# Kernel tuning notes

Hardware: AMD Instinct MI355X
Metric: run time of the kernel (lower is better)

## Reference

```python
import jax, jax.numpy as jnp
import numpy as np

N_NODES = 50000
N_EDGES = 800000
EPS = 1e-5


def _glorot(key, fan_in, fan_out):
    lim = np.sqrt(6.0 / (fan_in + fan_out))
    return jax.random.uniform(key, (fan_in, fan_out), jnp.float32, -lim, lim)


def setup_inputs() -> dict:
    key = jax.random.key(0)
    ks = jax.random.split(key, 16)
    x = jax.random.normal(ks[0], (N_NODES, 88), jnp.float32)
    edge_index = jax.random.randint(ks[1], (2, N_EDGES), 0, N_NODES, jnp.int64)
    dims = [(88, 70), (70, 60), (60, 50), (50, 60), (60, 70), (70, 88)]
    inp = {"x": x, "edge_index": edge_index}
    for i, (fi, fo) in enumerate(dims):
        inp[f"W{i+1}"] = _glorot(ks[2 + i], fi, fo)
        inp[f"b{i+1}"] = jnp.zeros((fo,), jnp.float32)
    # BatchNorm affine params for layers with bn: widths 70,60,60,70
    for i, w in enumerate([70, 60, 60, 70]):
        inp[f"g{i+1}"] = jnp.ones((w,), jnp.float32)
        inp[f"be{i+1}"] = jnp.zeros((w,), jnp.float32)
    return inp


def _gcn_norm(edge_index, n_nodes):
    # add self-loops, symmetric normalization: D^-1/2 (A+I) D^-1/2
    loop = jnp.arange(n_nodes, dtype=edge_index.dtype)
    src = jnp.concatenate([edge_index[0], loop])
    dst = jnp.concatenate([edge_index[1], loop])
    deg = jax.ops.segment_sum(jnp.ones_like(dst, jnp.float32), dst, num_segments=n_nodes)
    dis = jnp.where(deg > 0, jax.lax.rsqrt(deg), 0.0)
    norm = dis[src] * dis[dst]  # [E+N]
    return src, dst, norm


def _gcn(x, W, b, src, dst, norm, n_nodes):
    h = x @ W  # transform first (small out dim)
    msg = h[src] * norm[:, None]
    return jax.ops.segment_sum(msg, dst, num_segments=n_nodes) + b


def _bn(x, g, be):
    mu = jnp.mean(x, axis=0)
    var = jnp.mean(jnp.square(x - mu), axis=0)
    return g * (x - mu) * jax.lax.rsqrt(var + EPS) + be


def reference(x, edge_index, W1, b1, W2, b2, W3, b3, W4, b4, W5, b5, W6, b6,
              g1, be1, g2, be2, g3, be3, g4, be4):
    n = x.shape[0]
    src, dst, norm = _gcn_norm(edge_index, n)
    # encoder
    h = jax.nn.relu(_gcn(x, W1, b1, src, dst, norm, n))
    h = _bn(h, g1, be1)
    h = jax.nn.relu(_gcn(h, W2, b2, src, dst, norm, n))
    h = _bn(h, g2, be2)
    h = _gcn(h, W3, b3, src, dst, norm, n)
    # decoder
    h = jax.nn.relu(_gcn(h, W4, b4, src, dst, norm, n))
    h = _bn(h, g3, be3)
    h = jax.nn.relu(_gcn(h, W5, b5, src, dst, norm, n))
    h = _bn(h, g4, be4)
    h = _gcn(h, W6, b6, src, dst, norm, n)
    return h
```

## Files before the change

### kernel.cpp

```cpp
#include <hip/hip_runtime.h>
#include <hip/hip_bf16.h>

typedef unsigned int  uint_t;
typedef unsigned short ushort_t;

#define NN 50000
#define NE 800000
#define NBLK 196

static inline int cdiv(long long a, long long b) { return (int)((a + b - 1) / b); }

__device__ inline float bflo(uint_t u) { return __uint_as_float(u << 16); }
__device__ inline float bfhi(uint_t u) { return __uint_as_float(u & 0xffff0000u); }
__device__ inline uint_t packbf(float x, float y) {
    uint_t xu = __float_as_uint(x), yu = __float_as_uint(y);
    xu += 0x7fffu + ((xu >> 16) & 1u);
    yu += 0x7fffu + ((yu >> 16) & 1u);
    return (xu >> 16) | (yu & 0xffff0000u);
}
__device__ inline ushort_t packbf1(float x) {
    uint_t xu = __float_as_uint(x);
    xu += 0x7fffu + ((xu >> 16) & 1u);
    return (ushort_t)(xu >> 16);
}


__global__ void k_prep(int* __restrict__ deg, float* __restrict__ bnacc) {
    int i = blockIdx.x * blockDim.x + threadIdx.x;
    if (i < NN) deg[i] = 0;
    if (i < 768) bnacc[i] = 0.0f;
}

__global__ void k_hist(const int* __restrict__ dst, int* __restrict__ deg) {
    int e = blockIdx.x * blockDim.x + threadIdx.x;
    if (e < NE) {
        int d = dst[e];
        if ((unsigned)d < NN) atomicAdd(&deg[d], 1);
    }
}

__global__ void k_bsum(const int* __restrict__ deg, int* __restrict__ bsum) {
    __shared__ int l[256];
    int tid = threadIdx.x;
    int i = blockIdx.x * 256 + tid;
    l[tid] = (i < NN) ? deg[i] : 0;
    __syncthreads();
    for (int o = 128; o > 0; o >>= 1) {
        if (tid < o) l[tid] += l[tid + o];
        __syncthreads();
    }
    if (tid == 0) bsum[blockIdx.x] = l[0];
}

__global__ void k_bscan(const int* __restrict__ bsum, int* __restrict__ boff,
                        int* __restrict__ row_ptr) {
    __shared__ int l[256];
    int tid = threadIdx.x;
    int v = (tid < NBLK) ? bsum[tid] : 0;
    l[tid] = v;
    __syncthreads();
    for (int o = 1; o < 256; o <<= 1) {
        int t = (tid >= o) ? l[tid - o] : 0;
        __syncthreads();
        l[tid] += t;
        __syncthreads();
    }
    boff[tid] = l[tid] - v;
    if (tid == 255) row_ptr[NN] = l[255];
}

__global__ void k_rowptr(const int* __restrict__ deg, const int* __restrict__ boff,
                         int* __restrict__ row_ptr, int* __restrict__ cursor,
                         float* __restrict__ dis) {
    __shared__ int l[256];
    int tid = threadIdx.x;
    int i = blockIdx.x * 256 + tid;
    int v = (i < NN) ? deg[i] : 0;
    l[tid] = v;
    __syncthreads();
    for (int o = 1; o < 256; o <<= 1) {
        int t = (tid >= o) ? l[tid - o] : 0;
        __syncthreads();
        l[tid] += t;
        __syncthreads();
    }
    if (i < NN) {
        int excl = boff[blockIdx.x] + l[tid] - v;
        row_ptr[i] = excl;
        cursor[i] = excl;
        dis[i] = rsqrtf((float)(v + 1));
    }
}

__global__ void k_fill(const int* __restrict__ src, const int* __restrict__ dst,
                       const float* __restrict__ dis,
                       int* __restrict__ cursor, int2* __restrict__ cw) {
    int e = blockIdx.x * blockDim.x + threadIdx.x;
    if (e < NE) {
        int s = src[e], d = dst[e];
        if ((unsigned)s < NN && (unsigned)d < NN) {
            int p = atomicAdd(&cursor[d], 1);
            cw[p] = make_int2(s, __float_as_int(dis[s] * dis[d]));
        }
    }
}

struct FoldJob {
    const float* W; const float* b;
    const float* bnacc; const float* g; const float* be;
    float* Wp; float* bf;
    int FI, FO, in_bn, out_b;
};
struct FoldJobs { FoldJob j[4]; };

__global__ void k_fold(FoldJobs jobs) {
    FoldJob J = jobs.j[blockIdx.x];
    const int FI = J.FI, FO = J.FO;
    const int NT = (FO + 15) / 16, FOP = 16 * NT;
    __shared__ float scl[96], shl[96];
    int tid = threadIdx.x;
    if (J.in_bn) {
        if (tid < FI) {
            const float inv_n = 1.0f / NN;
            float mu = J.bnacc[tid] * inv_n;
            float va = J.bnacc[96 + tid] * inv_n - mu * mu;
            float r  = rsqrtf(va + 1e-5f);
            float sc = J.g[tid] * r;
            scl[tid] = sc;
            shl[tid] = J.be[tid] - mu * sc;
        }
        __syncthreads();
    }
    for (int idx = tid; idx < FI * FOP; idx += 256) {
        int k = idx / FOP, j = idx - k * FOP;
        float w = (j < FO) ? J.W[k * FO + j] : 0.0f;
        if (J.in_bn) w *= scl[k];
        J.Wp[(k >> 1) * 2 * FOP + 2 * j + (k & 1)] = w;
    }
    if (tid < FOP) {
        float a = (J.out_b && tid < FO) ? J.b[tid] : 0.0f;
        if (J.in_bn && tid < FO) {
            for (int k = 0; k < FI; ++k) a = fmaf(shl[k], J.W[k * FO + tid], a);
        }
        J.bf[tid] = a;
    }
}

template<int FI, int FO, int IN_BN, int IN_F32, int OUT_F32, int OUT_BN>
__global__ __launch_bounds__(256)
void k_dense(const void* __restrict__ Xv, const float* __restrict__ Wp,
             const float* __restrict__ biasf, void* __restrict__ Hv,
             float* __restrict__ bnst) {
    constexpr int NT  = (FO + 15) / 16;
    constexpr int FOP = 16 * NT;
    constexpr int FIP = FI + 2;
    constexpr int KP  = FI / 2;

    __shared__ __align__(16) float xs[64 * FIP];
    __shared__ float ls[96], lq[96];

    int tid = threadIdx.x;
    int node0 = blockIdx.x * 64;

    if (OUT_BN) {
        if (tid < 96) { ls[tid] = 0.0f; lq[tid] = 0.0f; }
    }

    if (IN_F32) {
        for (int idx = tid; idx < 64 * FI; idx += 256) {
            int r = idx / FI, c = idx - r * FI;
            int n = node0 + r;
            float v = (n < NN) ? ((const float*)Xv)[(size_t)n * FI + c] : 0.0f;
            if (IN_BN) v = fmaxf(v, 0.0f);
            xs[r * FIP + c] = v;
        }
    } else {
        for (int idx = tid; idx < 64 * KP; idx += 256) {
            int r = idx / KP, c2 = idx - r * KP;
            int n = node0 + r;
            uint_t u = (n < NN) ? ((const uint_t*)Xv)[(size_t)n * KP + c2] : 0u;
            float f0 = bflo(u), f1 = bfhi(u);
            if (IN_BN) { f0 = fmaxf(f0, 0.0f); f1 = fmaxf(f1, 0.0f); }
            xs[r * FIP + 2 * c2]     = f0;
            xs[r * FIP + 2 * c2 + 1] = f1;
        }
    }
    __syncthreads();

    int ng = tid >> 4;
    int cg = tid & 15;

    float acc[4][NT];
    #pragma unroll
    for (int i = 0; i < 4; ++i)
        #pragma unroll
        for (int t = 0; t < NT; ++t) acc[i][t] = biasf[cg + 16 * t];

    #pragma unroll 2
    for (int k = 0; k < FI; k += 2) {
        float2 xv[4];
        #pragma unroll
        for (int i = 0; i < 4; ++i)
            xv[i] = *(const float2*)&xs[(ng + 16 * i) * FIP + k];
        const float* wrow = &Wp[(k >> 1) * 2 * FOP];
        #pragma unroll
        for (int t = 0; t < NT; ++t) {
            float2 w = *(const float2*)&wrow[2 * (cg + 16 * t)];
            #pragma unroll
            for (int i = 0; i < 4; ++i)
                acc[i][t] = fmaf(xv[i].y, w.y, fmaf(xv[i].x, w.x, acc[i][t]));
        }
    }

    if (OUT_BN) {
        #pragma unroll
        for (int t = 0; t < NT; ++t) {
            int j = cg + 16 * t;
            if (j < FO) {
                float ps = 0.0f, pq = 0.0f;
                #pragma unroll
                for (int i = 0; i < 4; ++i) {
                    if (node0 + ng + 16 * i < NN) {
                        float r = fmaxf(acc[i][t], 0.0f);
                        ps += r; pq += r * r;
                    }
                }
                atomicAdd(&ls[j], ps);
                atomicAdd(&lq[j], pq);
            }
        }
        __syncthreads();
        if (tid < FO) {
            atomicAdd(&bnst[tid], ls[tid]);
            atomicAdd(&bnst[96 + tid], lq[tid]);
        }
    }

    #pragma unroll
    for (int i = 0; i < 4; ++i) {
        int n = node0 + ng + 16 * i;
        if (n < NN) {
            #pragma unroll
            for (int t = 0; t < NT; ++t) {
                int j = cg + 16 * t;
                if (j < FO) {
                    if (OUT_F32) ((float*)Hv)[(size_t)n * FO + j] = acc[i][t];
                    else ((ushort_t*)Hv)[(size_t)n * FO + j] = packbf1(acc[i][t]);
                }
            }
        }
    }
}

template<int FO, int IN_BN, int OUT_BIAS, int OUT_BN>
__global__ void k_gather(const ushort_t* __restrict__ h, const int* __restrict__ row_ptr,
                         const int2* __restrict__ cw, const float* __restrict__ dis,
                         const float* __restrict__ bnacc, const float* __restrict__ g,
                         const float* __restrict__ be,
                         const float* __restrict__ b, ushort_t* __restrict__ A,
                         float* __restrict__ bnacc_out) {
    constexpr int F2 = FO / 2;
    __shared__ float ls[96], lq[96];
    int tid = threadIdx.x;
    if (OUT_BN) {
        if (tid < 96) { ls[tid] = 0.0f; lq[tid] = 0.0f; }
        __syncthreads();
    }

    int t0 = blockIdx.x * blockDim.x + tid;
    const int stride = gridDim.x * blockDim.x;
    int j2 = t0 % F2;
    int j = 2 * j2;

    float sc0 = 1.0f, sh0 = 0.0f, sc1 = 1.0f, sh1 = 0.0f;
    if (IN_BN) {
        const float inv_n = 1.0f / NN;
        float mu0 = bnacc[j] * inv_n;
        float va0 = bnacc[96 + j] * inv_n - mu0 * mu0;
        float r0  = rsqrtf(va0 + 1e-5f);
        sc0 = g[j] * r0; sh0 = be[j] - mu0 * sc0;
        float mu1 = bnacc[j + 1] * inv_n;
        float va1 = bnacc[96 + j + 1] * inv_n - mu1 * mu1;
        float r1  = rsqrtf(va1 + 1e-5f);
        sc1 = g[j + 1] * r1; sh1 = be[j + 1] - mu1 * sc1;
    }

    const uint_t* h2 = (const uint_t*)h + j2;
    float sx = 0.0f, qx = 0.0f, sy = 0.0f, qy = 0.0f;

    for (int t = t0; t < NN * F2; t += stride) {
        int i = t / F2;
        float di = dis[i];

        uint_t su = h2[(size_t)i * F2];
        float vx = bflo(su), vy = bfhi(su);
        if (IN_BN) { vx = fmaxf(vx, 0.0f) * sc0 + sh0; vy = fmaxf(vy, 0.0f) * sc1 + sh1; }
        float ax = vx * di * di;
        float ay = vy * di * di;

        int k = row_ptr[i], end = row_ptr[i + 1];

        for (; k + 16 <= end; k += 16) {
            uint_t uu[16]; float ww[16];
            #pragma unroll
            for (int q = 0; q < 16; ++q) {
                int2 c = cw[k + q];
                ww[q] = __int_as_float(c.y);
                uu[q] = h2[(size_t)c.x * F2];
            }
            #pragma unroll
            for (int q = 0; q < 16; ++q) {
                float tx = bflo(uu[q]), ty = bfhi(uu[q]);
                if (IN_BN) { tx = fmaxf(tx, 0.0f) * sc0 + sh0; ty = fmaxf(ty, 0.0f) * sc1 + sh1; }
                ax = fmaf(tx, ww[q], ax); ay = fmaf(ty, ww[q], ay);
            }
        }
        for (; k + 8 <= end; k += 8) {
            uint_t uu[8]; float ww[8];
            #pragma unroll
            for (int q = 0; q < 8; ++q) {
                int2 c = cw[k + q];
                ww[q] = __int_as_float(c.y);
                uu[q] = h2[(size_t)c.x * F2];
            }
            #pragma unroll
            for (int q = 0; q < 8; ++q) {
                float tx = bflo(uu[q]), ty = bfhi(uu[q]);
                if (IN_BN) { tx = fmaxf(tx, 0.0f) * sc0 + sh0; ty = fmaxf(ty, 0.0f) * sc1 + sh1; }
                ax = fmaf(tx, ww[q], ax); ay = fmaf(ty, ww[q], ay);
            }
        }
        for (; k + 4 <= end; k += 4) {
            uint_t uu[4]; float ww[4];
            #pragma unroll
            for (int q = 0; q < 4; ++q) {
                int2 c = cw[k + q];
                ww[q] = __int_as_float(c.y);
                uu[q] = h2[(size_t)c.x * F2];
            }
            #pragma unroll
            for (int q = 0; q < 4; ++q) {
                float tx = bflo(uu[q]), ty = bfhi(uu[q]);
                if (IN_BN) { tx = fmaxf(tx, 0.0f) * sc0 + sh0; ty = fmaxf(ty, 0.0f) * sc1 + sh1; }
                ax = fmaf(tx, ww[q], ax); ay = fmaf(ty, ww[q], ay);
            }
        }
        for (; k < end; ++k) {
            int2 c = cw[k];
            float w = __int_as_float(c.y);
            uint_t u = h2[(size_t)c.x * F2];
            float tx = bflo(u), ty = bfhi(u);
            if (IN_BN) { tx = fmaxf(tx, 0.0f) * sc0 + sh0; ty = fmaxf(ty, 0.0f) * sc1 + sh1; }
            ax = fmaf(tx, w, ax); ay = fmaf(ty, w, ay);
        }

        if (OUT_BIAS) { ax += b[j]; ay += b[j + 1]; }
        if (OUT_BN) {
            float rx = fmaxf(ax, 0.0f), ry = fmaxf(ay, 0.0f);
            sx += rx; qx += rx * rx;
            sy += ry; qy += ry * ry;
        }
        ((uint_t*)A)[(size_t)i * F2 + j2] = packbf(ax, ay);
    }

    if (OUT_BN) {
        atomicAdd(&ls[j], sx);     atomicAdd(&ls[j + 1], sy);
        atomicAdd(&lq[j], qx);     atomicAdd(&lq[j + 1], qy);
        __syncthreads();
        if (tid < FO) {
            atomicAdd(&bnacc_out[tid], ls[tid]);
            atomicAdd(&bnacc_out[96 + tid], lq[tid]);
        }
    }
}

extern "C" void kernel_launch(void* const* d_in, const int* in_sizes, int n_in,
                              void* d_out, int out_size, void* d_ws, size_t ws_size,
                              hipStream_t stream) {
    const float* x = (const float*)d_in[0];
    const int* ei = (const int*)d_in[1];
    const int* src = ei;
    const int* dst = ei + NE;
    const float* W1 = (const float*)d_in[2];  const float* b1 = (const float*)d_in[3];
    const float* W2 = (const float*)d_in[4];  const float* b2 = (const float*)d_in[5];
    const float* W3 = (const float*)d_in[6];  const float* b3 = (const float*)d_in[7];
    const float* W4 = (const float*)d_in[8];  const float* b4 = (const float*)d_in[9];
    const float* W5 = (const float*)d_in[10]; const float* b5 = (const float*)d_in[11];
    const float* W6 = (const float*)d_in[12]; const float* b6 = (const float*)d_in[13];
    const float* g1 = (const float*)d_in[14]; const float* be1 = (const float*)d_in[15];
    const float* g2 = (const float*)d_in[16]; const float* be2 = (const float*)d_in[17];
    const float* g3 = (const float*)d_in[18]; const float* be3 = (const float*)d_in[19];
    const float* g4 = (const float*)d_in[20]; const float* be4 = (const float*)d_in[21];

    int2* cw      = (int2*)d_ws;
    float* dis    = (float*)(cw + NE);
    float* bnacc  = dis + NN;
    float* Wp     = bnacc + 768;
    float* biasf  = Wp + 6 * 7040;
    int* deg      = (int*)(biasf + 6 * 96);
    int* row_ptr  = deg + NN;
    int* cursor   = row_ptr + NN + 1;
    int* bsum     = cursor + NN;
    int* boff     = bsum + 256;
    ushort_t* hB  = (ushort_t*)(boff + 256);
    ushort_t* aB  = hB + (size_t)NN * 70;
    float* out    = (float*)d_out;

    const int NB = 256;
    const int DGRID = cdiv(NN, 64);
    float* bn0 = bnacc;
    float* bn1 = bnacc + 192;
    float* bn2 = bnacc + 384;
    float* bn3 = bnacc + 576;
    float* WpL[6]; float* bfL[6];
    for (int i = 0; i < 6; ++i) { WpL[i] = Wp + i * 7040; bfL[i] = biasf + i * 96; }

    k_prep<<<cdiv(NN, NB), NB, 0, stream>>>(deg, bnacc);
    k_hist<<<cdiv(NE, NB), NB, 0, stream>>>(dst, deg);
    k_bsum<<<NBLK, 256, 0, stream>>>(deg, bsum);
    k_bscan<<<1, 256, 0, stream>>>(bsum, boff, row_ptr);
    k_rowptr<<<NBLK, 256, 0, stream>>>(deg, boff, row_ptr, cursor, dis);
    k_fill<<<cdiv(NE, NB), NB, 0, stream>>>(src, dst, dis, cursor, cw);

    {
        FoldJobs js;
        js.j[0] = {W1, nullptr, nullptr, nullptr, nullptr, WpL[0], bfL[0], 88, 70, 0, 0};
        js.j[1] = {W4, b4,      nullptr, nullptr, nullptr, WpL[3], bfL[3], 50, 60, 0, 1};
        js.j[2] = {W5, b5,      nullptr, nullptr, nullptr, WpL[4], bfL[4], 60, 70, 0, 1};
        js.j[3] = {W6, b6,      nullptr, nullptr, nullptr, WpL[5], bfL[5], 70, 88, 0, 1};
        k_fold<<<4, 256, 0, stream>>>(js);
    }

    k_dense<88, 70, 0, 1, 0, 0><<<DGRID, 256, 0, stream>>>(x, WpL[0], bfL[0], hB, nullptr);
    k_gather<70, 0, 1, 1><<<56 * 35, NB, 0, stream>>>(
        hB, row_ptr, cw, dis, nullptr, nullptr, nullptr, b1, aB, bn0);

    {
        FoldJobs js;
        js.j[0] = {W2, nullptr, bn0, g1, be1, WpL[1], bfL[1], 70, 60, 1, 0};
        k_fold<<<1, 256, 0, stream>>>(js);
    }
    k_dense<70, 60, 1, 0, 0, 0><<<DGRID, 256, 0, stream>>>(aB, WpL[1], bfL[1], hB, nullptr);
    k_gather<60, 0, 1, 1><<<56 * 30, NB, 0, stream>>>(
        hB, row_ptr, cw, dis, nullptr, nullptr, nullptr, b2, aB, bn1);

    {
        FoldJobs js;
        js.j[0] = {W3, nullptr, bn1, g2, be2, WpL[2], bfL[2], 60, 50, 1, 0};
        k_fold<<<1, 256, 0, stream>>>(js);
    }
    k_dense<60, 50, 1, 0, 0, 0><<<DGRID, 256, 0, stream>>>(aB, WpL[2], bfL[2], hB, nullptr);
    k_gather<50, 0, 1, 0><<<cdiv((long long)NN * 25, NB), NB, 0, stream>>>(
        hB, row_ptr, cw, dis, nullptr, nullptr, nullptr, b3, aB, nullptr);

    k_gather<50, 0, 0, 0><<<cdiv((long long)NN * 25, NB), NB, 0, stream>>>(
        aB, row_ptr, cw, dis, nullptr, nullptr, nullptr, nullptr, hB, nullptr);
    k_dense<50, 60, 0, 0, 0, 1><<<DGRID, 256, 0, stream>>>(hB, WpL[3], bfL[3], aB, bn2);

    k_gather<60, 1, 0, 0><<<cdiv((long long)NN * 30, NB), NB, 0, stream>>>(
        aB, row_ptr, cw, dis, bn2, g3, be3, nullptr, hB, nullptr);
    k_dense<60, 70, 0, 0, 0, 1><<<DGRID, 256, 0, stream>>>(hB, WpL[4], bfL[4], aB, bn3);

    k_gather<70, 1, 0, 0><<<cdiv((long long)NN * 35, NB), NB, 0, stream>>>(
        aB, row_ptr, cw, dis, bn3, g4, be4, nullptr, hB, nullptr);
    k_dense<70, 88, 0, 0, 1, 0><<<DGRID, 256, 0, stream>>>(hB, WpL[5], bfL[5], out, nullptr);
}
```

Before: 553.8 us.

## Chunk feature layout into 8 column slabs and compute edge weights on the fly

```diff
diff --git a/kernel.cpp b/kernel.cpp
--- a/kernel.cpp
+++ b/kernel.cpp
@@ -93,14 +93,13 @@
 }
 
 __global__ void k_fill(const int* __restrict__ src, const int* __restrict__ dst,
-                       const float* __restrict__ dis,
-                       int* __restrict__ cursor, int2* __restrict__ cw) {
+                       int* __restrict__ cursor, int* __restrict__ col) {
     int e = blockIdx.x * blockDim.x + threadIdx.x;
     if (e < NE) {
         int s = src[e], d = dst[e];
         if ((unsigned)s < NN && (unsigned)d < NN) {
             int p = atomicAdd(&cursor[d], 1);
-            cw[p] = make_int2(s, __float_as_int(dis[s] * dis[d]));
+            col[p] = s;
         }
     }
 }
@@ -146,7 +145,7 @@
     }
 }
 
-template<int FI, int FO, int IN_BN, int IN_F32, int OUT_F32, int OUT_BN>
+template<int FI, int FO, int IN_BN, int PRI, int PRO, int OUT_BN>
 __global__ __launch_bounds__(256)
 void k_dense(const void* __restrict__ Xv, const float* __restrict__ Wp,
              const float* __restrict__ biasf, void* __restrict__ Hv,
@@ -154,7 +153,6 @@
     constexpr int NT  = (FO + 15) / 16;
     constexpr int FOP = 16 * NT;
     constexpr int FIP = FI + 2;
-    constexpr int KP  = FI / 2;
 
     __shared__ __align__(16) float xs[64 * FIP];
     __shared__ float ls[96], lq[96];
@@ -166,7 +164,7 @@
         if (tid < 96) { ls[tid] = 0.0f; lq[tid] = 0.0f; }
     }
 
-    if (IN_F32) {
+    if (PRI == 0) {
         for (int idx = tid; idx < 64 * FI; idx += 256) {
             int r = idx / FI, c = idx - r * FI;
             int n = node0 + r;
@@ -175,14 +173,20 @@
             xs[r * FIP + c] = v;
         }
     } else {
-        for (int idx = tid; idx < 64 * KP; idx += 256) {
-            int r = idx / KP, c2 = idx - r * KP;
-            int n = node0 + r;
-            uint_t u = (n < NN) ? ((const uint_t*)Xv)[(size_t)n * KP + c2] : 0u;
+        constexpr int PRIc = PRI ? PRI : 1;
+        for (int idx = tid; idx < 8 * 64 * PRIc; idx += 256) {
+            int c   = idx / (64 * PRIc);
+            int rem = idx - c * 64 * PRIc;
+            int r   = rem / PRIc;
+            int p   = rem - r * PRIc;
+            int n   = node0 + r;
+            uint_t u = (n < NN)
+                ? ((const uint_t*)Xv)[(size_t)c * NN * PRIc + (size_t)n * PRIc + p] : 0u;
             float f0 = bflo(u), f1 = bfhi(u);
             if (IN_BN) { f0 = fmaxf(f0, 0.0f); f1 = fmaxf(f1, 0.0f); }
-            xs[r * FIP + 2 * c2]     = f0;
-            xs[r * FIP + 2 * c2 + 1] = f1;
+            int j = c * 2 * PRIc + 2 * p;
+            if (j < FI)     xs[r * FIP + j]     = f0;
+            if (j + 1 < FI) xs[r * FIP + j + 1] = f1;
         }
     }
     __syncthreads();
@@ -243,23 +247,30 @@
             #pragma unroll
             for (int t = 0; t < NT; ++t) {
                 int j = cg + 16 * t;
-                if (j < FO) {
-                    if (OUT_F32) ((float*)Hv)[(size_t)n * FO + j] = acc[i][t];
-                    else ((ushort_t*)Hv)[(size_t)n * FO + j] = packbf1(acc[i][t]);
+                if (PRO == 0) {
+                    if (j < FO) ((float*)Hv)[(size_t)n * FO + j] = acc[i][t];
+                } else {
+                    constexpr int PROc = PRO ? PRO : 1;
+                    int co = j / (2 * PROc);
+                    int w  = j - co * 2 * PROc;
+                    ((ushort_t*)Hv)[(size_t)co * NN * 2 * PROc + (size_t)n * 2 * PROc + w]
+                        = packbf1(acc[i][t]);
                 }
             }
         }
     }
 }
 
-template<int FO, int IN_BN, int OUT_BIAS, int OUT_BN>
-__global__ void k_gather(const ushort_t* __restrict__ h, const int* __restrict__ row_ptr,
-                         const int2* __restrict__ cw, const float* __restrict__ dis,
-                         const float* __restrict__ bnacc, const float* __restrict__ g,
-                         const float* __restrict__ be,
-                         const float* __restrict__ b, ushort_t* __restrict__ A,
-                         float* __restrict__ bnacc_out) {
-    constexpr int F2 = FO / 2;
+template<int FO, int PR, int IN_BN, int OUT_BIAS, int OUT_BN>
+__global__ __launch_bounds__(256)
+void k_gather(const uint_t* __restrict__ h, const int* __restrict__ row_ptr,
+              const int* __restrict__ col, const float* __restrict__ dis,
+              const float* __restrict__ bnacc, const float* __restrict__ g,
+              const float* __restrict__ be,
+              const float* __restrict__ b, uint_t* __restrict__ A,
+              float* __restrict__ bnacc_out) {
+    constexpr int NPB = 256 / PR;
+    constexpr int NBTOT = (NN + NPB - 1) / NPB;
     __shared__ float ls[96], lq[96];
     int tid = threadIdx.x;
     if (OUT_BN) {
@@ -267,36 +278,48 @@
         __syncthreads();
     }
 
-    int t0 = blockIdx.x * blockDim.x + tid;
-    const int stride = gridDim.x * blockDim.x;
-    int j2 = t0 % F2;
+    int chunk = blockIdx.x & 7;
+    int GB    = gridDim.x >> 3;
+    int ln = tid / PR, p = tid - ln * PR;
+    int j2 = chunk * PR + p;
     int j = 2 * j2;
 
-    float sc0 = 1.0f, sh0 = 0.0f, sc1 = 1.0f, sh1 = 0.0f;
+    float sc0 = 0.0f, sh0 = 0.0f, sc1 = 0.0f, sh1 = 0.0f;
     if (IN_BN) {
         const float inv_n = 1.0f / NN;
-        float mu0 = bnacc[j] * inv_n;
-        float va0 = bnacc[96 + j] * inv_n - mu0 * mu0;
-        float r0  = rsqrtf(va0 + 1e-5f);
-        sc0 = g[j] * r0; sh0 = be[j] - mu0 * sc0;
-        float mu1 = bnacc[j + 1] * inv_n;
-        float va1 = bnacc[96 + j + 1] * inv_n - mu1 * mu1;
-        float r1  = rsqrtf(va1 + 1e-5f);
-        sc1 = g[j + 1] * r1; sh1 = be[j + 1] - mu1 * sc1;
-    }
-
-    const uint_t* h2 = (const uint_t*)h + j2;
+        if (j < FO) {
+            float mu = bnacc[j] * inv_n;
+            float va = bnacc[96 + j] * inv_n - mu * mu;
+            float r  = rsqrtf(va + 1e-5f);
+            sc0 = g[j] * r; sh0 = be[j] - mu * sc0;
+        }
+        if (j + 1 < FO) {
+            float mu = bnacc[j + 1] * inv_n;
+            float va = bnacc[96 + j + 1] * inv_n - mu * mu;
+            float r  = rsqrtf(va + 1e-5f);
+            sc1 = g[j + 1] * r; sh1 = be[j + 1] - mu * sc1;
+        }
+    }
+    float bx = 0.0f, by = 0.0f;
+    if (OUT_BIAS) {
+        if (j < FO)     bx = b[j];
+        if (j + 1 < FO) by = b[j + 1];
+    }
+
+    const uint_t* hr = h + (size_t)chunk * NN * PR + p;
+    uint_t* Ar = A + (size_t)chunk * NN * PR + p;
     float sx = 0.0f, qx = 0.0f, sy = 0.0f, qy = 0.0f;
 
-    for (int t = t0; t < NN * F2; t += stride) {
-        int i = t / F2;
+    for (int nb = blockIdx.x >> 3; nb < NBTOT; nb += GB) {
+        int i = nb * NPB + ln;
+        if (ln >= NPB || i >= NN) continue;
         float di = dis[i];
 
-        uint_t su = h2[(size_t)i * F2];
+        uint_t su = hr[(size_t)i * PR];
         float vx = bflo(su), vy = bfhi(su);
         if (IN_BN) { vx = fmaxf(vx, 0.0f) * sc0 + sh0; vy = fmaxf(vy, 0.0f) * sc1 + sh1; }
-        float ax = vx * di * di;
-        float ay = vy * di * di;
+        float ax = vx * di * di + bx;
+        float ay = vy * di * di + by;
 
         int k = row_ptr[i], end = row_ptr[i + 1];
 
@@ -304,9 +327,9 @@
             uint_t uu[16]; float ww[16];
             #pragma unroll
             for (int q = 0; q < 16; ++q) {
-                int2 c = cw[k + q];
-                ww[q] = __int_as_float(c.y);
-                uu[q] = h2[(size_t)c.x * F2];
+                int c = col[k + q];
+                ww[q] = dis[c] * di;
+                uu[q] = hr[(size_t)c * PR];
             }
             #pragma unroll
             for (int q = 0; q < 16; ++q) {
@@ -319,9 +342,9 @@
             uint_t uu[8]; float ww[8];
             #pragma unroll
             for (int q = 0; q < 8; ++q) {
-                int2 c = cw[k + q];
-                ww[q] = __int_as_float(c.y);
-                uu[q] = h2[(size_t)c.x * F2];
+                int c = col[k + q];
+                ww[q] = dis[c] * di;
+                uu[q] = hr[(size_t)c * PR];
             }
             #pragma unroll
             for (int q = 0; q < 8; ++q) {
@@ -334,9 +357,9 @@
             uint_t uu[4]; float ww[4];
             #pragma unroll
             for (int q = 0; q < 4; ++q) {
-                int2 c = cw[k + q];
-                ww[q] = __int_as_float(c.y);
-                uu[q] = h2[(size_t)c.x * F2];
+                int c = col[k + q];
+                ww[q] = dis[c] * di;
+                uu[q] = hr[(size_t)c * PR];
             }
             #pragma unroll
             for (int q = 0; q < 4; ++q) {
@@ -346,26 +369,25 @@
             }
         }
         for (; k < end; ++k) {
-            int2 c = cw[k];
-            float w = __int_as_float(c.y);
-            uint_t u = h2[(size_t)c.x * F2];
+            int c = col[k];
+            float w = dis[c] * di;
+            uint_t u = hr[(size_t)c * PR];
             float tx = bflo(u), ty = bfhi(u);
             if (IN_BN) { tx = fmaxf(tx, 0.0f) * sc0 + sh0; ty = fmaxf(ty, 0.0f) * sc1 + sh1; }
             ax = fmaf(tx, w, ax); ay = fmaf(ty, w, ay);
         }
 
-        if (OUT_BIAS) { ax += b[j]; ay += b[j + 1]; }
         if (OUT_BN) {
             float rx = fmaxf(ax, 0.0f), ry = fmaxf(ay, 0.0f);
             sx += rx; qx += rx * rx;
             sy += ry; qy += ry * ry;
         }
-        ((uint_t*)A)[(size_t)i * F2 + j2] = packbf(ax, ay);
+        Ar[(size_t)i * PR] = packbf(ax, ay);
     }
 
     if (OUT_BN) {
-        atomicAdd(&ls[j], sx);     atomicAdd(&ls[j + 1], sy);
-        atomicAdd(&lq[j], qx);     atomicAdd(&lq[j + 1], qy);
+        if (j < FO)     { atomicAdd(&ls[j], sx);     atomicAdd(&lq[j], qx); }
+        if (j + 1 < FO) { atomicAdd(&ls[j + 1], sy); atomicAdd(&lq[j + 1], qy); }
         __syncthreads();
         if (tid < FO) {
             atomicAdd(&bnacc_out[tid], ls[tid]);
@@ -392,8 +414,8 @@
     const float* g3 = (const float*)d_in[18]; const float* be3 = (const float*)d_in[19];
     const float* g4 = (const float*)d_in[20]; const float* be4 = (const float*)d_in[21];
 
-    int2* cw      = (int2*)d_ws;
-    float* dis    = (float*)(cw + NE);
+    int* col      = (int*)d_ws;
+    float* dis    = (float*)(col + NE);
     float* bnacc  = dis + NN;
     float* Wp     = bnacc + 768;
     float* biasf  = Wp + 6 * 7040;
@@ -402,8 +424,8 @@
     int* cursor   = row_ptr + NN + 1;
     int* bsum     = cursor + NN;
     int* boff     = bsum + 256;
-    ushort_t* hB  = (ushort_t*)(boff + 256);
-    ushort_t* aB  = hB + (size_t)NN * 70;
+    uint_t* hB    = (uint_t*)(boff + 256);
+    uint_t* aB    = hB + (size_t)NN * 40;
     float* out    = (float*)d_out;
 
     const int NB = 256;
@@ -415,12 +437,15 @@
     float* WpL[6]; float* bfL[6];
     for (int i = 0; i < 6; ++i) { WpL[i] = Wp + i * 7040; bfL[i] = biasf + i * 96; }
 
+    const int G5 = 8 * 245;
+    const int G4 = 8 * 196;
+
     k_prep<<<cdiv(NN, NB), NB, 0, stream>>>(deg, bnacc);
     k_hist<<<cdiv(NE, NB), NB, 0, stream>>>(dst, deg);
     k_bsum<<<NBLK, 256, 0, stream>>>(deg, bsum);
     k_bscan<<<1, 256, 0, stream>>>(bsum, boff, row_ptr);
     k_rowptr<<<NBLK, 256, 0, stream>>>(deg, boff, row_ptr, cursor, dis);
-    k_fill<<<cdiv(NE, NB), NB, 0, stream>>>(src, dst, dis, cursor, cw);
+    k_fill<<<cdiv(NE, NB), NB, 0, stream>>>(src, dst, cursor, col);
 
     {
         FoldJobs js;
@@ -431,37 +456,37 @@
         k_fold<<<4, 256, 0, stream>>>(js);
     }
 
-    k_dense<88, 70, 0, 1, 0, 0><<<DGRID, 256, 0, stream>>>(x, WpL[0], bfL[0], hB, nullptr);
-    k_gather<70, 0, 1, 1><<<56 * 35, NB, 0, stream>>>(
-        hB, row_ptr, cw, dis, nullptr, nullptr, nullptr, b1, aB, bn0);
+    k_dense<88, 70, 0, 0, 5, 0><<<DGRID, 256, 0, stream>>>(x, WpL[0], bfL[0], hB, nullptr);
+    k_gather<70, 5, 0, 1, 1><<<G5, NB, 0, stream>>>(
+        hB, row_ptr, col, dis, nullptr, nullptr, nullptr, b1, aB, bn0);
 
     {
         FoldJobs js;
         js.j[0] = {W2, nullptr, bn0, g1, be1, WpL[1], bfL[1], 70, 60, 1, 0};
         k_fold<<<1, 256, 0, stream>>>(js);
     }
-    k_dense<70, 60, 1, 0, 0, 0><<<DGRID, 256, 0, stream>>>(aB, WpL[1], bfL[1], hB, nullptr);
-    k_gather<60, 0, 1, 1><<<56 * 30, NB, 0, stream>>>(
-        hB, row_ptr, cw, dis, nullptr, nullptr, nullptr, b2, aB, bn1);
+    k_dense<70, 60, 1, 5, 4, 0><<<DGRID, 256, 0, stream>>>(aB, WpL[1], bfL[1], hB, nullptr);
+    k_gather<60, 4, 0, 1, 1><<<G4, NB, 0, stream>>>(
+        hB, row_ptr, col, dis, nullptr, nullptr, nullptr, b2, aB, bn1);
 
     {
         FoldJobs js;
         js.j[0] = {W3, nullptr, bn1, g2, be2, WpL[2], bfL[2], 60, 50, 1, 0};
         k_fold<<<1, 256, 0, stream>>>(js);
     }
-    k_dense<60, 50, 1, 0, 0, 0><<<DGRID, 256, 0, stream>>>(aB, WpL[2], bfL[2], hB, nullptr);
-    k_gather<50, 0, 1, 0><<<cdiv((long long)NN * 25, NB), NB, 0, stream>>>(
-        hB, row_ptr, cw, dis, nullptr, nullptr, nullptr, b3, aB, nullptr);
-
-    k_gather<50, 0, 0, 0><<<cdiv((long long)NN * 25, NB), NB, 0, stream>>>(
-        aB, row_ptr, cw, dis, nullptr, nullptr, nullptr, nullptr, hB, nullptr);
-    k_dense<50, 60, 0, 0, 0, 1><<<DGRID, 256, 0, stream>>>(hB, WpL[3], bfL[3], aB, bn2);
-
-    k_gather<60, 1, 0, 0><<<cdiv((long long)NN * 30, NB), NB, 0, stream>>>(
-        aB, row_ptr, cw, dis, bn2, g3, be3, nullptr, hB, nullptr);
-    k_dense<60, 70, 0, 0, 0, 1><<<DGRID, 256, 0, stream>>>(hB, WpL[4], bfL[4], aB, bn3);
-
-    k_gather<70, 1, 0, 0><<<cdiv((long long)NN * 35, NB), NB, 0, stream>>>(
-        aB, row_ptr, cw, dis, bn3, g4, be4, nullptr, hB, nullptr);
-    k_dense<70, 88, 0, 0, 1, 0><<<DGRID, 256, 0, stream>>>(hB, WpL[5], bfL[5], out, nullptr);
-}
+    k_dense<60, 50, 1, 4, 4, 0><<<DGRID, 256, 0, stream>>>(aB, WpL[2], bfL[2], hB, nullptr);
+    k_gather<50, 4, 0, 1, 0><<<G4, NB, 0, stream>>>(
+        hB, row_ptr, col, dis, nullptr, nullptr, nullptr, b3, aB, nullptr);
+
+    k_gather<50, 4, 0, 0, 0><<<G4, NB, 0, stream>>>(
+        aB, row_ptr, col, dis, nullptr, nullptr, nullptr, nullptr, hB, nullptr);
+    k_dense<50, 60, 0, 4, 4, 1><<<DGRID, 256, 0, stream>>>(hB, WpL[3], bfL[3], aB, bn2);
+
+    k_gather<60, 4, 1, 0, 0><<<G4, NB, 0, stream>>>(
+        aB, row_ptr, col, dis, bn2, g3, be3, nullptr, hB, nullptr);
+    k_dense<60, 70, 0, 4, 5, 1><<<DGRID, 256, 0, stream>>>(hB, WpL[4], bfL[4], aB, bn3);
+
+    k_gather<70, 5, 1, 0, 0><<<G5, NB, 0, stream>>>(
+        aB, row_ptr, col, dis, bn3, g4, be4, nullptr, hB, nullptr);
+    k_dense<70, 88, 0, 5, 0, 0><<<DGRID, 256, 0, stream>>>(hB, WpL[5], bfL[5], out, nullptr);
+}
```

After: 806.6 us. 1.46x slower.
